# Optimization experiments

Measured on AMD Instinct MI355X. Metric: run time of the kernel, lower is better.

Reference implementation:

```python
import jax, jax.numpy as jnp
import numpy as np

K = 1024
D = 256
BETA = 0.25


def setup_inputs() -> dict:
    key = jax.random.key(0)
    k1, k2 = jax.random.split(key)
    latents = jax.random.normal(k1, (32, D, 32, 32), dtype=jnp.float32)
    # nn.Embedding init: uniform(-1/K, 1/K)
    embedding = jax.random.uniform(k2, (K, D), dtype=jnp.float32,
                                   minval=-1.0 / K, maxval=1.0 / K)
    return {"latents": latents, "embedding": embedding}


def reference(latents, embedding):
    # latents: [B, D, H, W] -> [B, H, W, D]
    x = jnp.transpose(latents, (0, 2, 3, 1))
    input_shape = x.shape
    flat = x.reshape(-1, D)  # [N, D]

    # squared-L2 distances to codebook: [N, K]
    distances = (jnp.sum(flat ** 2, axis=1, keepdims=True)
                 + jnp.sum(embedding ** 2, axis=1)
                 - 2.0 * flat @ embedding.T)
    encoding_indices = jnp.argmin(distances, axis=1)  # [N]

    # one-hot encodings (returned output); quantize via direct gather
    encodings = jax.nn.one_hot(encoding_indices, K, dtype=latents.dtype)  # [N, K]
    quantized = embedding[encoding_indices].reshape(input_shape)  # [B, H, W, D]

    e_latent_loss = jnp.mean((jax.lax.stop_gradient(quantized) - x) ** 2)
    q_latent_loss = jnp.mean((quantized - jax.lax.stop_gradient(x)) ** 2)
    loss = q_latent_loss + BETA * e_latent_loss

    # straight-through estimator
    quantized_st = x + jax.lax.stop_gradient(quantized - x)

    avg_probs = jnp.mean(encodings, axis=0)  # [K]
    perplexity = jnp.exp(-jnp.sum(avg_probs * jnp.log(avg_probs + 1e-10)))

    return (loss,
            jnp.transpose(quantized_st, (0, 3, 1, 2)),  # [B, D, H, W]
            perplexity,
            encodings)
```

## Files before the change

### kernel.cpp

```cpp
#include <hip/hip_runtime.h>
#include <stdint.h>
#include <math.h>

typedef float  f32x4 __attribute__((ext_vector_type(4)));
typedef float  f32x2 __attribute__((ext_vector_type(2)));
typedef short  s16x8 __attribute__((ext_vector_type(8)));
typedef short  s16x4 __attribute__((ext_vector_type(4)));

#define KC   1024
#define DD   256
#define NR   32768

#define WS_HIST   0
#define WS_ACC    4096
#define WS_E2     8192
#define WS_IDX    12288
#define WS_PANEL  143360
#define WS_PART   671744

#define ENC_OFF   8388610ULL

#define A_OFF   0
#define B_OFF   32768
#define E2_OFF  65536
#define SMEM_SZ 67584

#define GLD16(gp, lp) __builtin_amdgcn_global_load_lds(                      \
    (const __attribute__((address_space(1))) uint32_t*)(gp),                 \
    (__attribute__((address_space(3))) uint32_t*)(lp), 16, 0, 0)

#define WAITVM(N) asm volatile("s_waitcnt vmcnt(" #N ")" ::: "memory")
#define PHASEBAR() do { __builtin_amdgcn_s_barrier();                        \
                        __builtin_amdgcn_sched_barrier(0); } while (0)

__device__ __forceinline__ short f2bf(float f) {
    uint32_t u = __builtin_bit_cast(uint32_t, f);
    uint32_t r = (u + 0x7FFFu + ((u >> 16) & 1u)) >> 16;
    return (short)r;
}

__global__ void k_prep(const float* __restrict__ emb, char* __restrict__ ws) {
    int tid = threadIdx.x;
    if (blockIdx.x == 0) {
        uint32_t* hist = (uint32_t*)(ws + WS_HIST);
        #pragma unroll
        for (int j = 0; j < 4; j++) hist[tid * 4 + j] = 0u;
        if (tid < 2) ((float*)(ws + WS_ACC))[tid] = 0.f;
    }
    int wid = tid >> 6, lane = tid & 63;
    int code = blockIdx.x * 4 + wid;
    const float* row = emb + (size_t)code * DD;
    f32x4 v = *(const f32x4*)(row + lane * 4);
    uint32_t lo = (uint32_t)(uint16_t)f2bf(v.x) | ((uint32_t)(uint16_t)f2bf(v.y) << 16);
    uint32_t hi = (uint32_t)(uint16_t)f2bf(v.z) | ((uint32_t)(uint16_t)f2bf(v.w) << 16);
    uint32_t* dst = (uint32_t*)((short*)(ws + WS_PANEL) + (size_t)code * DD + lane * 4);
    __builtin_nontemporal_store(lo, dst);
    __builtin_nontemporal_store(hi, dst + 1);
    float ss = v.x * v.x + v.y * v.y + v.z * v.z + v.w * v.w;
    #pragma unroll
    for (int off = 1; off < 64; off <<= 1) ss += __shfl_xor(ss, off);
    if (lane == 0)
        __builtin_nontemporal_store(ss, (float*)(ws + WS_E2) + code);
}

__global__ __launch_bounds__(256, 2) void k_argmin(const float* __restrict__ latents,
                                                   char* __restrict__ ws) {
    const char*  panelb = (const char*)(ws + WS_PANEL);
    const float* e2g    = (const float*)(ws + WS_E2);
    float*       acc    = (float*)(ws + WS_ACC);

    __shared__ __align__(16) char smem[SMEM_SZ];

    int t      = threadIdx.x;
    int lane   = t & 63;
    int wid    = t >> 6;
    int g      = lane >> 4, r16 = lane & 15;
    int rowgrp = blockIdx.x & 255;
    int chalf  = blockIdx.x >> 8;
    int nbase  = rowgrp * 128;
    int b      = nbase >> 10;
    int hwbase = nbase & 1023;
    int phase  = rowgrp & 31;
    const char* pbase = panelb + (size_t)chalf * 262144;

    if (t < 128) {
        f32x4 ev = *(const f32x4*)(e2g + chalf * 512 + t * 4);
        *(f32x4*)(smem + E2_OFF + t * 16) = ev;
    }

    float xs = 0.f;
    s16x8 af[2][8];
    int rg = (t & 15) * 4;
    int dp = (t >> 4) * 2;

    #pragma unroll
    for (int h = 0; h < 2; h++) {
        const float* base = latents + (size_t)b * 262144 + hwbase + h * 64 + rg;
        #pragma unroll
        for (int i = 0; i < 8; i++) {
            int d = dp + i * 32;
            f32x4 v0 = *(const f32x4*)(base + (size_t)d * 1024);
            f32x4 v1 = *(const f32x4*)(base + (size_t)(d + 1) * 1024);
            xs += v0.x*v0.x + v0.y*v0.y + v0.z*v0.z + v0.w*v0.w;
            xs += v1.x*v1.x + v1.y*v1.y + v1.z*v1.z + v1.w*v1.w;
            int qb = d >> 3;
            #pragma unroll
            for (int q = 0; q < 4; q++) {
                int slot = rg + q;
                uint32_t pk = (uint32_t)(uint16_t)f2bf(v0[q])
                            | ((uint32_t)(uint16_t)f2bf(v1[q]) << 16);
                int quad = qb ^ (slot & 7) ^ ((slot >> 3) & 7);
                *(uint32_t*)(smem + A_OFF + slot * 512 + quad * 16 + (d & 6) * 2) = pk;
            }
        }
        __syncthreads();
        if ((wid >> 1) == h) {
            int slotbase = (wid & 1) * 32;
            #pragma unroll
            for (int rt = 0; rt < 2; rt++) {
                #pragma unroll
                for (int kt = 0; kt < 8; kt++) {
                    int slot = slotbase + rt * 16 + r16;
                    int quad = (kt * 4 + g) ^ (slot & 7) ^ ((slot >> 3) & 7);
                    af[rt][kt] = *(const s16x8*)(smem + A_OFF + slot * 512 + quad * 16);
                }
            }
        }
        __syncthreads();
    }
    if (chalf == 0) {
        #pragma unroll
        for (int off = 1; off < 64; off <<= 1) xs += __shfl_xor(xs, off);
        if (lane == 0) atomicAdd(acc + 0, xs);
    }

    float vmin[2][4];
    int   vidx[2][4];
    #pragma unroll
    for (int rt = 0; rt < 2; rt++)
        #pragma unroll
        for (int j = 0; j < 4; j++) { vmin[rt][j] = 3.4e38f; vidx[rt][j] = 0; }

    const float* E2l = (const float*)(smem + E2_OFF);
    int codeglob = chalf * 512;

    auto stage = [&](int c) {
        const char* srcc = pbase + (size_t)c * 8192;
        char* dstb = smem + B_OFF + (size_t)(c & 3) * 8192;
        #pragma unroll
        for (int i = 0; i < 2; i++) {
            uint32_t off = i * 4096 + wid * 1024;
            uint32_t so  = off + lane * 16;
            uint32_t ssw = so ^ (((so >> 9) & 7u) << 4);
            GLD16(srcc + ssw, dstb + off);
        }
    };
    auto compute = [&](int c) {
        int cbase = c * 16;
        float e2c = E2l[cbase + r16];
        const char* Bc = smem + B_OFF + (size_t)(c & 3) * 8192;
        s16x8 bf[8];
        #pragma unroll
        for (int kt = 0; kt < 8; kt++) {
            uint32_t byte = (uint32_t)(r16 * 512)
                          + (((uint32_t)(kt * 64 + g * 16)) ^ (((uint32_t)(r16 & 7)) << 4));
            bf[kt] = *(const s16x8*)(Bc + byte);
        }
        #pragma unroll
        for (int rt = 0; rt < 2; rt++) {
            f32x4 a4 = {0.f, 0.f, 0.f, 0.f};
            #pragma unroll
            for (int kt = 0; kt < 8; kt++)
                a4 = __builtin_amdgcn_mfma_f32_16x16x32_bf16(af[rt][kt], bf[kt], a4, 0, 0, 0);
            #pragma unroll
            for (int j = 0; j < 4; j++) {
                float s = e2c - 2.f * a4[j];
                bool better = s < vmin[rt][j];
                vmin[rt][j] = better ? s : vmin[rt][j];
                vidx[rt][j] = better ? (codeglob + cbase + r16) : vidx[rt][j];
            }
        }
    };

    stage(phase); stage((phase + 1) & 31); stage((phase + 2) & 31);
    #pragma unroll 1
    for (int c = 0; c < 29; ++c) {
        WAITVM(4);
        PHASEBAR();
        compute((c + phase) & 31);
        stage((c + 3 + phase) & 31);
    }
    WAITVM(4); PHASEBAR(); compute((29 + phase) & 31);
    WAITVM(2); PHASEBAR(); compute((30 + phase) & 31);
    WAITVM(0); PHASEBAR(); compute((31 + phase) & 31);

    uint2* part = (uint2*)(ws + WS_PART) + (size_t)chalf * NR;
    #pragma unroll
    for (int rt = 0; rt < 2; rt++) {
        #pragma unroll
        for (int j = 0; j < 4; j++) {
            float s = vmin[rt][j]; int ii = vidx[rt][j];
            #pragma unroll
            for (int off = 1; off < 16; off <<= 1) {
                float os = __shfl_xor(s, off);
                int   oi = __shfl_xor(ii, off);
                if (os < s || (os == s && oi < ii)) { s = os; ii = oi; }
            }
            if (r16 == 0) {
                int n = nbase + wid * 32 + rt * 16 + g * 4 + j;
                uint2 pv;
                pv.x = __builtin_bit_cast(uint32_t, s);
                pv.y = (uint32_t)ii;
                part[n] = pv;
            }
        }
    }
}

__global__ void k_comb(char* __restrict__ ws) {
    const uint2* part = (const uint2*)(ws + WS_PART);
    uint32_t* hist = (uint32_t*)(ws + WS_HIST);
    float*    acc  = (float*)(ws + WS_ACC);
    int*      idxo = (int*)(ws + WS_IDX);
    int n = blockIdx.x * 256 + threadIdx.x;
    uint2 p0 = part[n];
    uint2 p1 = part[NR + n];
    float s0 = __builtin_bit_cast(float, p0.x);
    float s1 = __builtin_bit_cast(float, p1.x);
    float s = (s1 < s0) ? s1 : s0;
    int  ii = (s1 < s0) ? (int)p1.y : (int)p0.y;
    idxo[n] = ii;
    atomicAdd(hist + ii, 1u);
    #pragma unroll
    for (int off = 1; off < 64; off <<= 1) s += __shfl_xor(s, off);
    if ((threadIdx.x & 63) == 0) atomicAdd(acc + 1, s);
}

__global__ void k_quant(const float* __restrict__ emb, const char* __restrict__ ws,
                        float* __restrict__ out) {
    const int* idx = (const int*)(ws + WS_IDX);
    int tid = threadIdx.x;
    int dg  = blockIdx.x & 63;
    int hwt = (blockIdx.x >> 6) & 3;
    int b   = blockIdx.x >> 8;
    int hw  = hwt * 256 + tid;
    int n   = b * 1024 + hw;
    int code = idx[n];
    f32x4 v = *(const f32x4*)(emb + (size_t)code * 256 + dg * 4);
    float* dst = out + 1 + (size_t)b * 262144 + (size_t)dg * 4096 + hw;
    dst[0] = v.x; dst[1024] = v.y; dst[2048] = v.z; dst[3072] = v.w;
}

__global__ void k_onehot(const char* __restrict__ ws, float* __restrict__ out) {
    const int* idx = (const int*)(ws + WS_IDX);
    __shared__ int lidx[8];
    int tid = threadIdx.x;
    int rbase = blockIdx.x * 8;
    if (tid < 8) lidx[tid] = idx[rbase + tid];
    __syncthreads();
    f32x2* enc = (f32x2*)(out + ENC_OFF);
    #pragma unroll
    for (int j = 0; j < 16; j++) {
        int linear = j * 256 + tid;
        int rl = linear >> 9, c2 = linear & 511;
        int id = lidx[rl];
        f32x2 v;
        v.x = (2 * c2     == id) ? 1.f : 0.f;
        v.y = (2 * c2 + 1 == id) ? 1.f : 0.f;
        enc[(size_t)(rbase + rl) * 512 + c2] = v;
    }
}

__global__ void k_final(const char* __restrict__ ws, float* __restrict__ out) {
    __shared__ float red[256];
    const uint32_t* hist = (const uint32_t*)(ws + WS_HIST);
    const float*    acc  = (const float*)(ws + WS_ACC);
    int tid = threadIdx.x;
    float part = 0.f;
    #pragma unroll
    for (int j = 0; j < 4; j++) {
        float p = (float)hist[tid * 4 + j] * (1.f / 32768.f);
        part += p * logf(p + 1e-10f);
    }
    red[tid] = part;
    __syncthreads();
    for (int s = 128; s > 0; s >>= 1) {
        if (tid < s) red[tid] += red[tid + s];
        __syncthreads();
    }
    if (tid == 0) {
        out[8388609] = expf(-red[0]);
        out[0] = 1.25f * (acc[0] + acc[1]) * (1.f / 8388608.f);
    }
}

extern "C" void kernel_launch(void* const* d_in, const int* in_sizes, int n_in,
                              void* d_out, int out_size, void* d_ws, size_t ws_size,
                              hipStream_t stream) {
    const float* latents = (const float*)d_in[0];
    const float* emb     = (const float*)d_in[1];
    float* out = (float*)d_out;
    char*  ws  = (char*)d_ws;

    hipLaunchKernelGGL(k_prep,   dim3(256),  dim3(256), 0, stream, emb, ws);
    hipLaunchKernelGGL(k_argmin, dim3(512),  dim3(256), 0, stream, latents, ws);
    hipLaunchKernelGGL(k_comb,   dim3(128),  dim3(256), 0, stream, ws);
    hipLaunchKernelGGL(k_quant,  dim3(8192), dim3(256), 0, stream, emb, ws, out);
    hipLaunchKernelGGL(k_onehot, dim3(4096), dim3(256), 0, stream, ws, out);
    hipLaunchKernelGGL(k_final,  dim3(1),    dim3(256), 0, stream, ws, out);
}
```

Measured before the change: 89.55 us.

## Use per-wave private codebook staging and replicate bf16 panel across copies

Each wave now streams the whole codebook chunk into its own double-buffered LDS region and syncs only with its own waitcnts. This removes the block-wide barriers from the argmin main loop. The bf16 codebook panel is also written in 8 copies, and blocks pick a copy by block index to spread L2 and channel load. In exchange, each block moves four times as much global-to-LDS data, and the prep kernel writes eight times more panel data.

```diff
diff --git a/kernel.cpp b/kernel.cpp
--- a/kernel.cpp
+++ b/kernel.cpp
@@ -5,7 +5,6 @@
 typedef float  f32x4 __attribute__((ext_vector_type(4)));
 typedef float  f32x2 __attribute__((ext_vector_type(2)));
 typedef short  s16x8 __attribute__((ext_vector_type(8)));
-typedef short  s16x4 __attribute__((ext_vector_type(4)));
 
 #define KC   1024
 #define DD   256
@@ -16,12 +15,12 @@
 #define WS_E2     8192
 #define WS_IDX    12288
 #define WS_PANEL  143360
-#define WS_PART   671744
+#define WS_PART   4337664
 
 #define ENC_OFF   8388610ULL
 
 #define A_OFF   0
-#define B_OFF   32768
+#define B_OFF   0
 #define E2_OFF  65536
 #define SMEM_SZ 67584
 
@@ -29,9 +28,8 @@
     (const __attribute__((address_space(1))) uint32_t*)(gp),                 \
     (__attribute__((address_space(3))) uint32_t*)(lp), 16, 0, 0)
 
-#define WAITVM(N) asm volatile("s_waitcnt vmcnt(" #N ")" ::: "memory")
-#define PHASEBAR() do { __builtin_amdgcn_s_barrier();                        \
-                        __builtin_amdgcn_sched_barrier(0); } while (0)
+#define WAITVM(N)  asm volatile("s_waitcnt vmcnt(" #N ")" ::: "memory")
+#define WAITLGKM() asm volatile("s_waitcnt lgkmcnt(0)" ::: "memory")
 
 __device__ __forceinline__ short f2bf(float f) {
     uint32_t u = __builtin_bit_cast(uint32_t, f);
@@ -41,6 +39,8 @@
 
 __global__ void k_prep(const float* __restrict__ emb, char* __restrict__ ws) {
     int tid = threadIdx.x;
+    int cb   = blockIdx.x & 255;
+    int copy = blockIdx.x >> 8;
     if (blockIdx.x == 0) {
         uint32_t* hist = (uint32_t*)(ws + WS_HIST);
         #pragma unroll
@@ -48,19 +48,22 @@
         if (tid < 2) ((float*)(ws + WS_ACC))[tid] = 0.f;
     }
     int wid = tid >> 6, lane = tid & 63;
-    int code = blockIdx.x * 4 + wid;
+    int code = cb * 4 + wid;
     const float* row = emb + (size_t)code * DD;
     f32x4 v = *(const f32x4*)(row + lane * 4);
     uint32_t lo = (uint32_t)(uint16_t)f2bf(v.x) | ((uint32_t)(uint16_t)f2bf(v.y) << 16);
     uint32_t hi = (uint32_t)(uint16_t)f2bf(v.z) | ((uint32_t)(uint16_t)f2bf(v.w) << 16);
-    uint32_t* dst = (uint32_t*)((short*)(ws + WS_PANEL) + (size_t)code * DD + lane * 4);
+    uint32_t* dst = (uint32_t*)((short*)(ws + WS_PANEL)
+                  + (size_t)copy * 262144 + (size_t)code * DD + lane * 4);
     __builtin_nontemporal_store(lo, dst);
     __builtin_nontemporal_store(hi, dst + 1);
-    float ss = v.x * v.x + v.y * v.y + v.z * v.z + v.w * v.w;
-    #pragma unroll
-    for (int off = 1; off < 64; off <<= 1) ss += __shfl_xor(ss, off);
-    if (lane == 0)
-        __builtin_nontemporal_store(ss, (float*)(ws + WS_E2) + code);
+    if (copy == 0) {
+        float ss = v.x * v.x + v.y * v.y + v.z * v.z + v.w * v.w;
+        #pragma unroll
+        for (int off = 1; off < 64; off <<= 1) ss += __shfl_xor(ss, off);
+        if (lane == 0)
+            __builtin_nontemporal_store(ss, (float*)(ws + WS_E2) + code);
+    }
 }
 
 __global__ __launch_bounds__(256, 2) void k_argmin(const float* __restrict__ latents,
@@ -81,7 +84,8 @@
     int b      = nbase >> 10;
     int hwbase = nbase & 1023;
     int phase  = rowgrp & 31;
-    const char* pbase = panelb + (size_t)chalf * 262144;
+    const char* pbase = panelb + (size_t)(blockIdx.x & 7) * 524288
+                      + (size_t)chalf * 262144;
 
     if (t < 128) {
         f32x4 ev = *(const f32x4*)(e2g + chalf * 512 + t * 4);
@@ -143,29 +147,40 @@
 
     const float* E2l = (const float*)(smem + E2_OFF);
     int codeglob = chalf * 512;
-
-    auto stage = [&](int c) {
-        const char* srcc = pbase + (size_t)c * 8192;
-        char* dstb = smem + B_OFF + (size_t)(c & 3) * 8192;
-        #pragma unroll
-        for (int i = 0; i < 2; i++) {
-            uint32_t off = i * 4096 + wid * 1024;
-            uint32_t so  = off + lane * 16;
+    char* mybuf = smem + B_OFF + wid * 16384;
+    uint32_t lsw = (uint32_t)(lane * 16);
+    uint32_t bfoff[8];
+    #pragma unroll
+    for (int kt = 0; kt < 8; kt++)
+        bfoff[kt] = (uint32_t)(r16 * 512)
+                  + (((uint32_t)(kt * 64 + g * 16)) ^ (((uint32_t)(r16 & 7)) << 4));
+
+    auto stage = [&](int cc, int par) {
+        const char* srcc = pbase + (size_t)cc * 8192;
+        char* dstb = mybuf + par * 8192;
+        #pragma unroll
+        for (int i = 0; i < 8; i++) {
+            uint32_t so  = (uint32_t)(i * 1024) + lsw;
             uint32_t ssw = so ^ (((so >> 9) & 7u) << 4);
-            GLD16(srcc + ssw, dstb + off);
+            GLD16(srcc + ssw, dstb + i * 1024);
         }
     };
-    auto compute = [&](int c) {
-        int cbase = c * 16;
+
+    int c0 = phase & 31, c1 = (phase + 1) & 31;
+    stage(c0, c0 & 1);
+    stage(c1, c1 & 1);
+    #pragma unroll 1
+    for (int c = 0; c < 32; ++c) {
+        int cc = (c + phase) & 31;
+        WAITVM(8);
+        const char* Bc = mybuf + (cc & 1) * 8192;
+        s16x8 bf[8];
+        #pragma unroll
+        for (int kt = 0; kt < 8; kt++) bf[kt] = *(const s16x8*)(Bc + bfoff[kt]);
+        WAITLGKM();
+        if (c < 30) { int cn = (c + 2 + phase) & 31; stage(cn, cn & 1); }
+        int cbase = cc * 16;
         float e2c = E2l[cbase + r16];
-        const char* Bc = smem + B_OFF + (size_t)(c & 3) * 8192;
-        s16x8 bf[8];
-        #pragma unroll
-        for (int kt = 0; kt < 8; kt++) {
-            uint32_t byte = (uint32_t)(r16 * 512)
-                          + (((uint32_t)(kt * 64 + g * 16)) ^ (((uint32_t)(r16 & 7)) << 4));
-            bf[kt] = *(const s16x8*)(Bc + byte);
-        }
         #pragma unroll
         for (int rt = 0; rt < 2; rt++) {
             f32x4 a4 = {0.f, 0.f, 0.f, 0.f};
@@ -180,19 +195,7 @@
                 vidx[rt][j] = better ? (codeglob + cbase + r16) : vidx[rt][j];
             }
         }
-    };
-
-    stage(phase); stage((phase + 1) & 31); stage((phase + 2) & 31);
-    #pragma unroll 1
-    for (int c = 0; c < 29; ++c) {
-        WAITVM(4);
-        PHASEBAR();
-        compute((c + phase) & 31);
-        stage((c + 3 + phase) & 31);
-    }
-    WAITVM(4); PHASEBAR(); compute((29 + phase) & 31);
-    WAITVM(2); PHASEBAR(); compute((30 + phase) & 31);
-    WAITVM(0); PHASEBAR(); compute((31 + phase) & 31);
+    }
 
     uint2* part = (uint2*)(ws + WS_PART) + (size_t)chalf * NR;
     #pragma unroll
@@ -302,7 +305,7 @@
     float* out = (float*)d_out;
     char*  ws  = (char*)d_ws;
 
-    hipLaunchKernelGGL(k_prep,   dim3(256),  dim3(256), 0, stream, emb, ws);
+    hipLaunchKernelGGL(k_prep,   dim3(2048), dim3(256), 0, stream, emb, ws);
     hipLaunchKernelGGL(k_argmin, dim3(512),  dim3(256), 0, stream, latents, ws);
     hipLaunchKernelGGL(k_comb,   dim3(128),  dim3(256), 0, stream, ws);
     hipLaunchKernelGGL(k_quant,  dim3(8192), dim3(256), 0, stream, emb, ws, out);
```

Result: slower. 92.67 us (+3.5%).
